# Kernel tuning notes

Measured on AMD Instinct MI355X. Metric: run time of the kernel, lower is better.

The kernel has to match this reference:

```python
import jax, jax.numpy as jnp
import numpy as np

N = 100000
E = 1600000
D = 128      # in_features
H = 128      # mlp hidden = out_features
O = 128      # out_features
BN_EPS = 1e-5

def _bn_train(x, gamma, beta):
    # BatchNorm1d in training mode: batch stats over node axis, biased variance
    mu = jnp.mean(x, axis=0)
    var = jnp.mean((x - mu) ** 2, axis=0)
    return (x - mu) * jax.lax.rsqrt(var + BN_EPS) * gamma + beta

def setup_inputs() -> dict:
    key = jax.random.key(0)
    ks = jax.random.split(key, 8)
    h = jax.random.normal(ks[0], (N, D), dtype=jnp.float32)
    edge_src = jax.random.randint(ks[1], (E,), 0, N, dtype=jnp.int32)
    edge_dst = jax.random.randint(ks[2], (E,), 0, N, dtype=jnp.int32)
    s1 = 1.0 / np.sqrt(D)
    s2 = 1.0 / np.sqrt(H)
    W1 = jax.random.uniform(ks[3], (D, H), jnp.float32, -s1, s1)
    b1 = jax.random.uniform(ks[4], (H,), jnp.float32, -s1, s1)
    W2 = jax.random.uniform(ks[5], (H, O), jnp.float32, -s2, s2)
    b2 = jax.random.uniform(ks[6], (O,), jnp.float32, -s2, s2)
    return {
        "h": h, "edge_src": edge_src, "edge_dst": edge_dst,
        "W1": W1, "b1": b1, "g1": jnp.ones((H,), jnp.float32), "be1": jnp.zeros((H,), jnp.float32),
        "W2": W2, "b2": b2, "g2": jnp.ones((O,), jnp.float32), "be2": jnp.zeros((O,), jnp.float32),
        "eps": jnp.zeros((), jnp.float32),
    }

def reference(h, edge_src, edge_dst, W1, b1, g1, be1, W2, b2, g2, be2, eps):
    # spmm(Adj, h) == scatter-add of gathered neighbor features
    msgs = h[edge_src]                                   # [E, D] irregular gather
    pooled = jax.ops.segment_sum(msgs, edge_dst, num_segments=N)  # [N, D]
    pooled = pooled + (1.0 + eps) * h                    # eps combine
    # MLP (2 layers): Linear -> BN -> ReLU -> Linear
    x = jax.nn.relu(_bn_train(pooled @ W1 + b1, g1, be1))
    x = x @ W2 + b2
    # final BN + ReLU
    return jax.nn.relu(_bn_train(x, g2, be2))
```

## Files before the change

kernel.cpp:

```cpp
#include <hip/hip_runtime.h>
#include <hip/hip_bf16.h>
#include <stdint.h>

#define BN_EPS 1e-5f

typedef __attribute__((ext_vector_type(8)))  short bf16x8;
typedef __attribute__((ext_vector_type(16))) float f32x16;

static __device__ __forceinline__ float bflo2f(uint32_t p){
  union { uint32_t u; float f; } c; c.u = p << 16; return c.f;
}
static __device__ __forceinline__ float bfhi2f(uint32_t p){
  union { uint32_t u; float f; } c; c.u = p & 0xffff0000u; return c.f;
}
static __device__ __forceinline__ uint16_t f2bf(float f){
  union { float f; uint32_t u; } c; c.f = f;
  uint32_t u = c.u;
  return (uint16_t)((u + 0x7fffu + ((u >> 16) & 1u)) >> 16);
}
static __device__ __forceinline__ uint32_t pack2(float a, float b){
  return (uint32_t)f2bf(a) | ((uint32_t)f2bf(b) << 16);
}

__global__ void k_prep(const float* __restrict__ h, uint16_t* __restrict__ hb, int hblocks,
                       const float* __restrict__ W1, const float* __restrict__ W2,
                       uint16_t* __restrict__ Wt1, uint16_t* __restrict__ Wt2){
  if ((int)blockIdx.x < hblocks){
    int i = (blockIdx.x * 256 + threadIdx.x) * 8;
    float4 a = *(const float4*)(h + i);
    float4 b = *(const float4*)(h + i + 4);
    uint4 o;
    o.x = pack2(a.x, a.y); o.y = pack2(a.z, a.w);
    o.z = pack2(b.x, b.y); o.w = pack2(b.z, b.w);
    *(uint4*)(hb + i) = o;
    return;
  }
  int gid = (blockIdx.x - hblocks) * 256 + threadIdx.x;
  if (gid >= 4096) return;
  const float* Wf = (gid < 2048) ? W1 : W2;
  uint16_t* Wt = (gid < 2048) ? Wt1 : Wt2;
  int cid = gid & 2047;
  int nrow = cid >> 4;
  int c    = cid & 15;
  int k0 = c * 8;
  float e[8];
  #pragma unroll
  for (int j = 0; j < 8; ++j) e[j] = Wf[(k0 + j) * 128 + nrow];
  uint4 o;
  o.x = pack2(e[0], e[1]); o.y = pack2(e[2], e[3]);
  o.z = pack2(e[4], e[5]); o.w = pack2(e[6], e[7]);
  int cs = c ^ (nrow & 15);
  *(uint4*)(Wt + nrow * 128 + cs * 8) = o;
}

__global__ void k_bhist(const int* __restrict__ dst, int* __restrict__ M, int E, int NB){
  __shared__ int cnt[512];
  int t = threadIdx.x;
  cnt[t] = 0; cnt[t + 256] = 0;
  __syncthreads();
  int base = blockIdx.x * 4096;
  #pragma unroll 4
  for (int j = t; j < 4096; j += 256){
    int i = base + j;
    if (i < E) atomicAdd(&cnt[dst[i] >> 8], 1);
  }
  __syncthreads();
  size_t row = (size_t)blockIdx.x * NB;
  if (t < NB) M[row + t] = cnt[t];
  int t2 = t + 256;
  if (t2 < NB) M[row + t2] = cnt[t2];
}

__global__ void k_colscan(int* __restrict__ M, int* __restrict__ btot, int EB, int NB){
  __shared__ int s[256];
  int b = blockIdx.x, t = threadIdx.x;
  int i0 = 2 * t, i1 = 2 * t + 1;
  int v0 = (i0 < EB) ? M[(size_t)i0 * NB + b] : 0;
  int v1 = (i1 < EB) ? M[(size_t)i1 * NB + b] : 0;
  s[t] = v0 + v1;
  __syncthreads();
  for (int off = 1; off < 256; off <<= 1){
    int v = (t >= off) ? s[t - off] : 0;
    __syncthreads();
    s[t] += v;
    __syncthreads();
  }
  int excl = s[t] - (v0 + v1);
  if (i0 < EB) M[(size_t)i0 * NB + b] = excl;
  if (i1 < EB) M[(size_t)i1 * NB + b] = excl + v0;
  if (t == 255) btot[b] = s[255];
}

__global__ void k_bscan(const int* __restrict__ btot, int* __restrict__ bbase,
                        int* __restrict__ row_off, int NB, int n, int E){
  __shared__ int s[256];
  int t = threadIdx.x;
  int i0 = 2 * t, i1 = 2 * t + 1;
  int v0 = (i0 < NB) ? btot[i0] : 0;
  int v1 = (i1 < NB) ? btot[i1] : 0;
  s[t] = v0 + v1;
  __syncthreads();
  for (int off = 1; off < 256; off <<= 1){
    int v = (t >= off) ? s[t - off] : 0;
    __syncthreads();
    s[t] += v;
    __syncthreads();
  }
  int excl = s[t] - (v0 + v1);
  if (i0 < NB) bbase[i0] = excl;
  if (i1 < NB) bbase[i1] = excl + v0;
  if (t == 0){ bbase[NB] = E; row_off[n] = E; }
}

__global__ void k_bin(const int* __restrict__ src, const int* __restrict__ dst,
                      const int* __restrict__ M, const int* __restrict__ bbase,
                      uint2* __restrict__ binned, int E, int NB){
  __shared__ int comb[512];
  __shared__ int cur[512];
  int t = threadIdx.x;
  size_t row = (size_t)blockIdx.x * NB;
  if (t < NB) comb[t] = bbase[t] + M[row + t];
  int t2 = t + 256;
  if (t2 < NB) comb[t2] = bbase[t2] + M[row + t2];
  cur[t] = 0; cur[t + 256] = 0;
  __syncthreads();
  int base = blockIdx.x * 4096;
  #pragma unroll 4
  for (int j = t; j < 4096; j += 256){
    int i = base + j;
    if (i < E){
      int d = dst[i];
      int b = d >> 8;
      int r = atomicAdd(&cur[b], 1);
      binned[comb[b] + r] = make_uint2((unsigned)src[i], (unsigned)d);
    }
  }
}

__global__ void k_csr(const uint2* __restrict__ binned, const int* __restrict__ bbase,
                      int* __restrict__ row_off, int* __restrict__ col_idx, int n){
  __shared__ int cnt[256];
  __shared__ int off[256];
  __shared__ int cur[256];
  int b = blockIdx.x, t = threadIdx.x;
  int e0 = bbase[b], e1 = bbase[b + 1];
  int nb0 = b << 8;
  cnt[t] = 0; cur[t] = 0;
  __syncthreads();
  int m = e1 - e0;
  for (int j = t; j < m; j += 256) atomicAdd(&cnt[binned[e0 + j].y & 255], 1);
  __syncthreads();
  int v = cnt[t];
  off[t] = v;
  __syncthreads();
  for (int o = 1; o < 256; o <<= 1){
    int u = (t >= o) ? off[t - o] : 0;
    __syncthreads();
    off[t] += u;
    __syncthreads();
  }
  int excl = off[t] - v;
  __syncthreads();
  off[t] = excl;
  if (nb0 + t < n) row_off[nb0 + t] = e0 + excl;
  __syncthreads();
  for (int j = t; j < m; j += 256){
    uint2 p = binned[e0 + j];
    int dl = p.y & 255;
    int r = atomicAdd(&cur[dl], 1);
    col_idx[e0 + off[dl] + r] = (int)p.x;
  }
}

__global__ void k_gather(const uint16_t* __restrict__ hb, const int* __restrict__ row_off,
                         const int* __restrict__ col_idx, const float* __restrict__ eps_p,
                         uint16_t* __restrict__ Xb, int n){
  int node = (blockIdx.x << 2) + (threadIdx.x >> 6);
  int lane = threadIdx.x & 63;
  if (node >= n) return;
  int g = lane >> 4;
  int c = lane & 15;
  const uint4* hp4 = (const uint4*)hb;
  int j = row_off[node], jend = row_off[node + 1];
  float a0=0.f,a1=0.f,a2=0.f,a3=0.f,a4=0.f,a5=0.f,a6=0.f,a7=0.f;
  for (; j + 8 <= jend; j += 8){
    int sA = col_idx[j + g];
    int sB = col_idx[j + 4 + g];
    uint4 vA = hp4[(size_t)sA * 16 + c];
    uint4 vB = hp4[(size_t)sB * 16 + c];
    a0 += bflo2f(vA.x) + bflo2f(vB.x);
    a1 += bfhi2f(vA.x) + bfhi2f(vB.x);
    a2 += bflo2f(vA.y) + bflo2f(vB.y);
    a3 += bfhi2f(vA.y) + bfhi2f(vB.y);
    a4 += bflo2f(vA.z) + bflo2f(vB.z);
    a5 += bfhi2f(vA.z) + bfhi2f(vB.z);
    a6 += bflo2f(vA.w) + bflo2f(vB.w);
    a7 += bfhi2f(vA.w) + bfhi2f(vB.w);
  }
  for (; j + 4 <= jend; j += 4){
    int s = col_idx[j + g];
    uint4 v = hp4[(size_t)s * 16 + c];
    a0 += bflo2f(v.x); a1 += bfhi2f(v.x);
    a2 += bflo2f(v.y); a3 += bfhi2f(v.y);
    a4 += bflo2f(v.z); a5 += bfhi2f(v.z);
    a6 += bflo2f(v.w); a7 += bfhi2f(v.w);
  }
  int rem = jend - j;
  if (rem > 0){
    int jj = j + (g < rem ? g : rem - 1);
    float w = (g < rem) ? 1.f : 0.f;
    int s = col_idx[jj];
    uint4 v = hp4[(size_t)s * 16 + c];
    a0 = fmaf(w, bflo2f(v.x), a0); a1 = fmaf(w, bfhi2f(v.x), a1);
    a2 = fmaf(w, bflo2f(v.y), a2); a3 = fmaf(w, bfhi2f(v.y), a3);
    a4 = fmaf(w, bflo2f(v.z), a4); a5 = fmaf(w, bfhi2f(v.z), a5);
    a6 = fmaf(w, bflo2f(v.w), a6); a7 = fmaf(w, bfhi2f(v.w), a7);
  }
  a0 += __shfl_xor(a0, 16); a1 += __shfl_xor(a1, 16);
  a2 += __shfl_xor(a2, 16); a3 += __shfl_xor(a3, 16);
  a4 += __shfl_xor(a4, 16); a5 += __shfl_xor(a5, 16);
  a6 += __shfl_xor(a6, 16); a7 += __shfl_xor(a7, 16);
  a0 += __shfl_xor(a0, 32); a1 += __shfl_xor(a1, 32);
  a2 += __shfl_xor(a2, 32); a3 += __shfl_xor(a3, 32);
  a4 += __shfl_xor(a4, 32); a5 += __shfl_xor(a5, 32);
  a6 += __shfl_xor(a6, 32); a7 += __shfl_xor(a7, 32);
  if (g == 0){
    float ce = 1.0f + eps_p[0];
    uint4 vh = hp4[(size_t)node * 16 + c];
    a0 = fmaf(ce, bflo2f(vh.x), a0); a1 = fmaf(ce, bfhi2f(vh.x), a1);
    a2 = fmaf(ce, bflo2f(vh.y), a2); a3 = fmaf(ce, bfhi2f(vh.y), a3);
    a4 = fmaf(ce, bflo2f(vh.z), a4); a5 = fmaf(ce, bfhi2f(vh.z), a5);
    a6 = fmaf(ce, bflo2f(vh.w), a6); a7 = fmaf(ce, bfhi2f(vh.w), a7);
    uint4 o;
    o.x = pack2(a0, a1); o.y = pack2(a2, a3);
    o.z = pack2(a4, a5); o.w = pack2(a6, a7);
    *((uint4*)Xb + (size_t)node * 16 + c) = o;
  }
}

template<bool BN_IN>
__global__ __launch_bounds__(256, 3) void k_mgemm(
    const uint16_t* __restrict__ Ag, const uint16_t* __restrict__ Wt,
    const float* __restrict__ bias_f, const float* __restrict__ ABin,
    uint16_t* __restrict__ Yout, float* __restrict__ osum, float* __restrict__ osq, int n){
  __shared__ __align__(16) uint16_t Al[64 * 128];
  __shared__ __align__(16) uint16_t Wl[128 * 128];
  __shared__ float csum[128], csq[128];
  int tid = threadIdx.x;
  int rbase = blockIdx.x * 64;

  {
    const uint4* g = (const uint4*)Wt;
    uint4* d = (uint4*)Wl;
    #pragma unroll
    for (int i = 0; i < 8; ++i) d[tid + 256 * i] = g[tid + 256 * i];
  }
  #pragma unroll
  for (int i = 0; i < 4; ++i){
    int f = tid + 256 * i;
    int m = f >> 4, c = f & 15;
    int gr = rbase + m;
    uint4 v = make_uint4(0, 0, 0, 0);
    if (gr < n){
      v = *(const uint4*)(Ag + (size_t)gr * 128 + c * 8);
      if (BN_IN){
        int k0 = c * 8;
        float4 ka0 = *(const float4*)(ABin + k0);
        float4 ka1 = *(const float4*)(ABin + k0 + 4);
        float4 kb0 = *(const float4*)(ABin + 128 + k0);
        float4 kb1 = *(const float4*)(ABin + 128 + k0 + 4);
        float e0 = fmaxf(fmaf(bflo2f(v.x), ka0.x, kb0.x), 0.f);
        float e1 = fmaxf(fmaf(bfhi2f(v.x), ka0.y, kb0.y), 0.f);
        float e2 = fmaxf(fmaf(bflo2f(v.y), ka0.z, kb0.z), 0.f);
        float e3 = fmaxf(fmaf(bfhi2f(v.y), ka0.w, kb0.w), 0.f);
        float e4 = fmaxf(fmaf(bflo2f(v.z), ka1.x, kb1.x), 0.f);
        float e5 = fmaxf(fmaf(bfhi2f(v.z), ka1.y, kb1.y), 0.f);
        float e6 = fmaxf(fmaf(bflo2f(v.w), ka1.z, kb1.z), 0.f);
        float e7 = fmaxf(fmaf(bfhi2f(v.w), ka1.w, kb1.w), 0.f);
        v.x = pack2(e0, e1); v.y = pack2(e2, e3);
        v.z = pack2(e4, e5); v.w = pack2(e6, e7);
      }
    }
    *(uint4*)((char*)Al + m * 256 + ((c ^ (m & 15)) * 16)) = v;
  }
  if (tid < 128){ csum[tid] = 0.f; csq[tid] = 0.f; }
  __syncthreads();

  int lane = tid & 63;
  int w    = tid >> 6;
  int hi   = lane >> 5;
  int key  = lane & 15;
  int m0   = (w & 1) * 32;
  int n0   = (w >> 1) * 64;
  int mrow = m0 + (lane & 31);
  int nrow0 = n0 + (lane & 31);
  int nrow1 = nrow0 + 32;

  f32x16 acc0, acc1;
  #pragma unroll
  for (int i = 0; i < 16; ++i){ acc0[i] = 0.f; acc1[i] = 0.f; }

  const char* Ab = (const char*)Al;
  const char* Wb = (const char*)Wl;
  #pragma unroll
  for (int kt = 0; kt < 8; ++kt){
    int cs = ((2 * kt + hi) ^ key) * 16;
    bf16x8 a  = *(const bf16x8*)(Ab + mrow  * 256 + cs);
    bf16x8 b0 = *(const bf16x8*)(Wb + nrow0 * 256 + cs);
    bf16x8 b1 = *(const bf16x8*)(Wb + nrow1 * 256 + cs);
    acc0 = __builtin_amdgcn_mfma_f32_32x32x16_bf16(a, b0, acc0, 0, 0, 0);
    acc1 = __builtin_amdgcn_mfma_f32_32x32x16_bf16(a, b1, acc1, 0, 0, 0);
  }
  __syncthreads();

  uint16_t* Yl = Wl;
  float bias0 = bias_f[nrow0];
  float bias1 = bias_f[nrow1];
  float ps0 = 0.f, pq0 = 0.f, ps1 = 0.f, pq1 = 0.f;
  #pragma unroll
  for (int r = 0; r < 16; ++r){
    int row = m0 + (r & 3) + 8 * (r >> 2) + 4 * hi;
    bool valid = (rbase + row) < n;
    float y0 = acc0[r] + bias0;
    float y1 = acc1[r] + bias1;
    if (valid){
      ps0 += y0; pq0 += y0 * y0;
      ps1 += y1; pq1 += y1 * y1;
    }
    Yl[row * 128 + nrow0] = f2bf(y0);
    Yl[row * 128 + nrow1] = f2bf(y1);
  }
  atomicAdd(&csum[nrow0], ps0); atomicAdd(&csq[nrow0], pq0);
  atomicAdd(&csum[nrow1], ps1); atomicAdd(&csq[nrow1], pq1);
  __syncthreads();

  #pragma unroll
  for (int i = 0; i < 4; ++i){
    int id = tid + 256 * i;
    int row = id >> 4, c = id & 15;
    int gr = rbase + row;
    if (gr < n)
      *((uint4*)Yout + (size_t)gr * 16 + c) = *((const uint4*)Yl + id);
  }
  if (tid < 128){
    atomicAdd(&osum[tid], csum[tid]);
    atomicAdd(&osq[tid], csq[tid]);
  }
}

__global__ void k_bncoef(const float* __restrict__ sum, const float* __restrict__ sq,
                         const float* __restrict__ g, const float* __restrict__ be,
                         float* __restrict__ AB, float invN){
  int c = threadIdx.x;
  if (c < 128){
    float mu = sum[c] * invN;
    float var = sq[c] * invN - mu * mu;
    float A = g[c] * rsqrtf(var + BN_EPS);
    float B = be[c] - mu * A;
    AB[c] = A;
    AB[128 + c] = B;
  }
}

__global__ void k_final(const uint16_t* __restrict__ Y2b, const float* __restrict__ AB,
                        float* __restrict__ out, int total){
  int i = (blockIdx.x * 256 + threadIdx.x) * 4;
  if (i >= total) return;
  uint2 v = *(const uint2*)(Y2b + i);
  int c = i & 127;
  float4 a = *(const float4*)(AB + c);
  float4 b = *(const float4*)(AB + 128 + c);
  float4 o;
  o.x = fmaxf(fmaf(bflo2f(v.x), a.x, b.x), 0.f);
  o.y = fmaxf(fmaf(bfhi2f(v.x), a.y, b.y), 0.f);
  o.z = fmaxf(fmaf(bflo2f(v.y), a.z, b.z), 0.f);
  o.w = fmaxf(fmaf(bfhi2f(v.y), a.w, b.w), 0.f);
  *(float4*)(out + i) = o;
}

extern "C" void kernel_launch(void* const* d_in, const int* in_sizes, int n_in,
                              void* d_out, int out_size, void* d_ws, size_t ws_size,
                              hipStream_t stream){
  const float* h    = (const float*)d_in[0];
  const int*   esrc = (const int*)d_in[1];
  const int*   edst = (const int*)d_in[2];
  const float* W1   = (const float*)d_in[3];
  const float* b1   = (const float*)d_in[4];
  const float* g1   = (const float*)d_in[5];
  const float* be1  = (const float*)d_in[6];
  const float* W2   = (const float*)d_in[7];
  const float* b2   = (const float*)d_in[8];
  const float* g2   = (const float*)d_in[9];
  const float* be2  = (const float*)d_in[10];
  const float* eps  = (const float*)d_in[11];
  int n = in_sizes[0] / 128;
  int E = in_sizes[1];
  (void)n_in; (void)out_size; (void)ws_size;

  int NB = (n + 255) >> 8;
  int EB = (E + 4095) >> 12;

  char* ws = (char*)d_ws;
  size_t off = 0;
  auto alloc = [&](size_t bytes) -> void* {
    void* p = ws + off;
    off += (bytes + 511) & ~(size_t)511;
    return p;
  };
  size_t feat_b = (size_t)n * 128 * 2;
  uint16_t* B1   = (uint16_t*)alloc(feat_b);
  uint16_t* B2   = (uint16_t*)alloc(feat_b);
  int*   row_off = (int*)alloc((size_t)(n + 1) * 4);
  int*   col_idx = (int*)alloc((size_t)E * 4);
  int*   M       = (int*)alloc((size_t)EB * NB * 4);
  int*   btot    = (int*)alloc((size_t)(NB + 1) * 4);
  int*   bbase   = (int*)alloc((size_t)(NB + 1) * 4);
  float* stats   = (float*)alloc(512 * 4);
  float* AB1     = (float*)alloc(256 * 4);
  float* AB2     = (float*)alloc(256 * 4);
  uint16_t* Wt1  = (uint16_t*)alloc(128 * 128 * 2);
  uint16_t* Wt2  = (uint16_t*)alloc(128 * 128 * 2);
  float* sum1 = stats;        float* sq1 = stats + 128;
  float* sum2 = stats + 256;  float* sq2 = stats + 384;
  uint16_t* hb  = B1;
  uint2*   binned = (uint2*)B2;
  uint16_t* Xb  = B2;
  uint16_t* Y1b = B1;
  uint16_t* Y2b = B2;

  hipMemsetAsync(stats, 0, 512 * 4, stream);

  int total = n * 128;
  int hblocks = total / 8 / 256;
  k_prep<<<hblocks + 16, 256, 0, stream>>>(h, hb, hblocks, W1, W2, Wt1, Wt2);

  k_bhist  <<<EB, 256, 0, stream>>>(edst, M, E, NB);
  k_colscan<<<NB, 256, 0, stream>>>(M, btot, EB, NB);
  k_bscan  <<<1, 256, 0, stream>>>(btot, bbase, row_off, NB, n, E);
  k_bin    <<<EB, 256, 0, stream>>>(esrc, edst, M, bbase, binned, E, NB);
  k_csr    <<<NB, 256, 0, stream>>>(binned, bbase, row_off, col_idx, n);

  k_gather<<<(n + 3) / 4, 256, 0, stream>>>(hb, row_off, col_idx, eps, Xb, n);

  int gblocks = (n + 63) / 64;
  k_mgemm<false><<<gblocks, 256, 0, stream>>>(Xb, Wt1, b1, nullptr, Y1b, sum1, sq1, n);
  k_bncoef<<<1, 128, 0, stream>>>(sum1, sq1, g1, be1, AB1, 1.0f / (float)n);
  k_mgemm<true> <<<gblocks, 256, 0, stream>>>(Y1b, Wt2, b2, AB1, Y2b, sum2, sq2, n);
  k_bncoef<<<1, 128, 0, stream>>>(sum2, sq2, g2, be2, AB2, 1.0f / (float)n);

  k_final<<<(total / 4 + 255) / 256, 256, 0, stream>>>(Y2b, AB2, (float*)d_out, total);
}
```

Measured before the change: 361.0 us.

## Fuse CSR build into one persistent kernel with grid barriers, fold BN coefficients

Merges the five CSR-construction kernels into one kernel that separates its phases with a global atomic grid barrier. The BN coefficient kernels are removed and each GEMM/final block recomputes the coefficients in shared memory. The stats memset moves into k_prep, and the gather loop is unrolled to 16 edges per iteration for more memory-level parallelism. The goal is to cut launch overhead and tiny serial kernels. The grid barrier assumes all NG (~391) blocks are co-resident, which risks deadlock if occupancy is insufficient.

```diff
diff --git a/kernel.cpp b/kernel.cpp
--- a/kernel.cpp
+++ b/kernel.cpp
@@ -24,7 +24,16 @@
 
 __global__ void k_prep(const float* __restrict__ h, uint16_t* __restrict__ hb, int hblocks,
                        const float* __restrict__ W1, const float* __restrict__ W2,
-                       uint16_t* __restrict__ Wt1, uint16_t* __restrict__ Wt2){
+                       uint16_t* __restrict__ Wt1, uint16_t* __restrict__ Wt2,
+                       float* __restrict__ stats, int* __restrict__ bar){
+  if (blockIdx.x == gridDim.x - 1){
+    if (threadIdx.x < 128){
+      float4 z = make_float4(0.f, 0.f, 0.f, 0.f);
+      *(float4*)(stats + threadIdx.x * 4) = z;
+    } else if (threadIdx.x == 128){
+      *bar = 0;
+    }
+  }
   if ((int)blockIdx.x < hblocks){
     int i = (blockIdx.x * 256 + threadIdx.x) * 8;
     float4 a = *(const float4*)(h + i);
@@ -53,122 +62,131 @@
   *(uint4*)(Wt + nrow * 128 + cs * 8) = o;
 }
 
-__global__ void k_bhist(const int* __restrict__ dst, int* __restrict__ M, int E, int NB){
-  __shared__ int cnt[512];
-  int t = threadIdx.x;
-  cnt[t] = 0; cnt[t + 256] = 0;
+static __device__ __forceinline__ void gridbar(int* bar, int nblocks, int phase){
   __syncthreads();
-  int base = blockIdx.x * 4096;
-  #pragma unroll 4
-  for (int j = t; j < 4096; j += 256){
-    int i = base + j;
-    if (i < E) atomicAdd(&cnt[dst[i] >> 8], 1);
+  if (threadIdx.x == 0){
+    __hip_atomic_fetch_add(bar, 1, __ATOMIC_RELEASE, __HIP_MEMORY_SCOPE_AGENT);
+    int target = nblocks * phase;
+    while (__hip_atomic_load(bar, __ATOMIC_ACQUIRE, __HIP_MEMORY_SCOPE_AGENT) < target){
+      __builtin_amdgcn_s_sleep(8);
+    }
   }
   __syncthreads();
-  size_t row = (size_t)blockIdx.x * NB;
-  if (t < NB) M[row + t] = cnt[t];
-  int t2 = t + 256;
-  if (t2 < NB) M[row + t2] = cnt[t2];
-}
-
-__global__ void k_colscan(int* __restrict__ M, int* __restrict__ btot, int EB, int NB){
-  __shared__ int s[256];
+}
+
+__global__ __launch_bounds__(256, 4) void k_csr_all(
+    const int* __restrict__ src, const int* __restrict__ dst,
+    int* __restrict__ M, int* __restrict__ btot, int* __restrict__ bbase,
+    int* __restrict__ row_off, int* __restrict__ col_idx, uint2* __restrict__ binned,
+    int* __restrict__ bar, int E, int n, int NB, int EB, int NG){
+  __shared__ int sm[1024];
   int b = blockIdx.x, t = threadIdx.x;
-  int i0 = 2 * t, i1 = 2 * t + 1;
-  int v0 = (i0 < EB) ? M[(size_t)i0 * NB + b] : 0;
-  int v1 = (i1 < EB) ? M[(size_t)i1 * NB + b] : 0;
-  s[t] = v0 + v1;
-  __syncthreads();
-  for (int off = 1; off < 256; off <<= 1){
-    int v = (t >= off) ? s[t - off] : 0;
-    __syncthreads();
-    s[t] += v;
-    __syncthreads();
-  }
-  int excl = s[t] - (v0 + v1);
-  if (i0 < EB) M[(size_t)i0 * NB + b] = excl;
-  if (i1 < EB) M[(size_t)i1 * NB + b] = excl + v0;
-  if (t == 255) btot[b] = s[255];
-}
-
-__global__ void k_bscan(const int* __restrict__ btot, int* __restrict__ bbase,
-                        int* __restrict__ row_off, int NB, int n, int E){
-  __shared__ int s[256];
-  int t = threadIdx.x;
-  int i0 = 2 * t, i1 = 2 * t + 1;
-  int v0 = (i0 < NB) ? btot[i0] : 0;
-  int v1 = (i1 < NB) ? btot[i1] : 0;
-  s[t] = v0 + v1;
-  __syncthreads();
-  for (int off = 1; off < 256; off <<= 1){
-    int v = (t >= off) ? s[t - off] : 0;
-    __syncthreads();
-    s[t] += v;
-    __syncthreads();
-  }
-  int excl = s[t] - (v0 + v1);
-  if (i0 < NB) bbase[i0] = excl;
-  if (i1 < NB) bbase[i1] = excl + v0;
-  if (t == 0){ bbase[NB] = E; row_off[n] = E; }
-}
-
-__global__ void k_bin(const int* __restrict__ src, const int* __restrict__ dst,
-                      const int* __restrict__ M, const int* __restrict__ bbase,
-                      uint2* __restrict__ binned, int E, int NB){
-  __shared__ int comb[512];
-  __shared__ int cur[512];
-  int t = threadIdx.x;
-  size_t row = (size_t)blockIdx.x * NB;
-  if (t < NB) comb[t] = bbase[t] + M[row + t];
-  int t2 = t + 256;
-  if (t2 < NB) comb[t2] = bbase[t2] + M[row + t2];
-  cur[t] = 0; cur[t + 256] = 0;
-  __syncthreads();
-  int base = blockIdx.x * 4096;
-  #pragma unroll 4
-  for (int j = t; j < 4096; j += 256){
-    int i = base + j;
-    if (i < E){
-      int d = dst[i];
-      int b = d >> 8;
-      int r = atomicAdd(&cur[b], 1);
-      binned[comb[b] + r] = make_uint2((unsigned)src[i], (unsigned)d);
-    }
-  }
-}
-
-__global__ void k_csr(const uint2* __restrict__ binned, const int* __restrict__ bbase,
-                      int* __restrict__ row_off, int* __restrict__ col_idx, int n){
-  __shared__ int cnt[256];
-  __shared__ int off[256];
-  __shared__ int cur[256];
-  int b = blockIdx.x, t = threadIdx.x;
-  int e0 = bbase[b], e1 = bbase[b + 1];
-  int nb0 = b << 8;
-  cnt[t] = 0; cur[t] = 0;
-  __syncthreads();
-  int m = e1 - e0;
-  for (int j = t; j < m; j += 256) atomicAdd(&cnt[binned[e0 + j].y & 255], 1);
-  __syncthreads();
-  int v = cnt[t];
-  off[t] = v;
-  __syncthreads();
-  for (int o = 1; o < 256; o <<= 1){
-    int u = (t >= o) ? off[t - o] : 0;
-    __syncthreads();
-    off[t] += u;
-    __syncthreads();
-  }
-  int excl = off[t] - v;
-  __syncthreads();
-  off[t] = excl;
-  if (nb0 + t < n) row_off[nb0 + t] = e0 + excl;
-  __syncthreads();
-  for (int j = t; j < m; j += 256){
-    uint2 p = binned[e0 + j];
-    int dl = p.y & 255;
-    int r = atomicAdd(&cur[dl], 1);
-    col_idx[e0 + off[dl] + r] = (int)p.x;
+
+  if (b < EB){
+    sm[t] = 0; sm[t + 256] = 0;
+    __syncthreads();
+    int base = b * 4096;
+    #pragma unroll 4
+    for (int j = t; j < 4096; j += 256){
+      int i = base + j;
+      if (i < E) atomicAdd(&sm[dst[i] >> 8], 1);
+    }
+    __syncthreads();
+    size_t row = (size_t)b * NB;
+    if (t < NB) M[row + t] = sm[t];
+    int t2 = t + 256;
+    if (t2 < NB) M[row + t2] = sm[t2];
+  }
+  gridbar(bar, NG, 1);
+
+  if (b < NB){
+    int i0 = 2 * t, i1 = 2 * t + 1;
+    int v0 = (i0 < EB) ? M[(size_t)i0 * NB + b] : 0;
+    int v1 = (i1 < EB) ? M[(size_t)i1 * NB + b] : 0;
+    sm[t] = v0 + v1;
+    __syncthreads();
+    for (int off = 1; off < 256; off <<= 1){
+      int v = (t >= off) ? sm[t - off] : 0;
+      __syncthreads();
+      sm[t] += v;
+      __syncthreads();
+    }
+    int excl = sm[t] - (v0 + v1);
+    if (i0 < EB) M[(size_t)i0 * NB + b] = excl;
+    if (i1 < EB) M[(size_t)i1 * NB + b] = excl + v0;
+    if (t == 255) btot[b] = sm[255];
+  }
+  gridbar(bar, NG, 2);
+
+  if (b == 0){
+    int i0 = 2 * t, i1 = 2 * t + 1;
+    int v0 = (i0 < NB) ? btot[i0] : 0;
+    int v1 = (i1 < NB) ? btot[i1] : 0;
+    sm[t] = v0 + v1;
+    __syncthreads();
+    for (int off = 1; off < 256; off <<= 1){
+      int v = (t >= off) ? sm[t - off] : 0;
+      __syncthreads();
+      sm[t] += v;
+      __syncthreads();
+    }
+    int excl = sm[t] - (v0 + v1);
+    if (i0 < NB) bbase[i0] = excl;
+    if (i1 < NB) bbase[i1] = excl + v0;
+    if (t == 0){ bbase[NB] = E; row_off[n] = E; }
+  }
+  gridbar(bar, NG, 3);
+
+  if (b < EB){
+    size_t row = (size_t)b * NB;
+    if (t < NB) sm[t] = bbase[t] + M[row + t];
+    int t2 = t + 256;
+    if (t2 < NB) sm[t2] = bbase[t2] + M[row + t2];
+    sm[512 + t] = 0; sm[768 + t] = 0;
+    __syncthreads();
+    int base = b * 4096;
+    #pragma unroll 4
+    for (int j = t; j < 4096; j += 256){
+      int i = base + j;
+      if (i < E){
+        int d = dst[i];
+        int bk = d >> 8;
+        int r = atomicAdd(&sm[512 + bk], 1);
+        binned[sm[bk] + r] = make_uint2((unsigned)src[i], (unsigned)d);
+      }
+    }
+  }
+  gridbar(bar, NG, 4);
+
+  if (b < NB){
+    int e0 = bbase[b], e1 = bbase[b + 1];
+    int nb0 = b << 8;
+    sm[t] = 0;
+    sm[512 + t] = 0;
+    __syncthreads();
+    int m = e1 - e0;
+    for (int j = t; j < m; j += 256) atomicAdd(&sm[binned[e0 + j].y & 255], 1);
+    __syncthreads();
+    int v = sm[t];
+    sm[256 + t] = v;
+    __syncthreads();
+    for (int o = 1; o < 256; o <<= 1){
+      int u = (t >= o) ? sm[256 + t - o] : 0;
+      __syncthreads();
+      sm[256 + t] += u;
+      __syncthreads();
+    }
+    int excl = sm[256 + t] - v;
+    __syncthreads();
+    sm[256 + t] = excl;
+    if (nb0 + t < n) row_off[nb0 + t] = e0 + excl;
+    __syncthreads();
+    for (int j = t; j < m; j += 256){
+      uint2 p = binned[e0 + j];
+      int dl = p.y & 255;
+      int r = atomicAdd(&sm[512 + dl], 1);
+      col_idx[e0 + sm[256 + dl] + r] = (int)p.x;
+    }
   }
 }
 
@@ -183,6 +201,24 @@
   const uint4* hp4 = (const uint4*)hb;
   int j = row_off[node], jend = row_off[node + 1];
   float a0=0.f,a1=0.f,a2=0.f,a3=0.f,a4=0.f,a5=0.f,a6=0.f,a7=0.f;
+  for (; j + 16 <= jend; j += 16){
+    int sA = col_idx[j + g];
+    int sB = col_idx[j + 4 + g];
+    int sC = col_idx[j + 8 + g];
+    int sD = col_idx[j + 12 + g];
+    uint4 vA = hp4[(size_t)sA * 16 + c];
+    uint4 vB = hp4[(size_t)sB * 16 + c];
+    uint4 vC = hp4[(size_t)sC * 16 + c];
+    uint4 vD = hp4[(size_t)sD * 16 + c];
+    a0 += (bflo2f(vA.x) + bflo2f(vB.x)) + (bflo2f(vC.x) + bflo2f(vD.x));
+    a1 += (bfhi2f(vA.x) + bfhi2f(vB.x)) + (bfhi2f(vC.x) + bfhi2f(vD.x));
+    a2 += (bflo2f(vA.y) + bflo2f(vB.y)) + (bflo2f(vC.y) + bflo2f(vD.y));
+    a3 += (bfhi2f(vA.y) + bfhi2f(vB.y)) + (bfhi2f(vC.y) + bfhi2f(vD.y));
+    a4 += (bflo2f(vA.z) + bflo2f(vB.z)) + (bflo2f(vC.z) + bflo2f(vD.z));
+    a5 += (bfhi2f(vA.z) + bfhi2f(vB.z)) + (bfhi2f(vC.z) + bfhi2f(vD.z));
+    a6 += (bflo2f(vA.w) + bflo2f(vB.w)) + (bflo2f(vC.w) + bflo2f(vD.w));
+    a7 += (bfhi2f(vA.w) + bfhi2f(vB.w)) + (bfhi2f(vC.w) + bfhi2f(vD.w));
+  }
   for (; j + 8 <= jend; j += 8){
     int sA = col_idx[j + g];
     int sB = col_idx[j + 4 + g];
@@ -241,13 +277,27 @@
 template<bool BN_IN>
 __global__ __launch_bounds__(256, 3) void k_mgemm(
     const uint16_t* __restrict__ Ag, const uint16_t* __restrict__ Wt,
-    const float* __restrict__ bias_f, const float* __restrict__ ABin,
+    const float* __restrict__ bias_f,
+    const float* __restrict__ sin, const float* __restrict__ sqin,
+    const float* __restrict__ gin, const float* __restrict__ bein, float invN,
     uint16_t* __restrict__ Yout, float* __restrict__ osum, float* __restrict__ osq, int n){
   __shared__ __align__(16) uint16_t Al[64 * 128];
   __shared__ __align__(16) uint16_t Wl[128 * 128];
   __shared__ float csum[128], csq[128];
+  __shared__ __align__(16) float ABl[256];
   int tid = threadIdx.x;
   int rbase = blockIdx.x * 64;
+
+  if (BN_IN){
+    if (tid < 128){
+      float mu = sin[tid] * invN;
+      float var = sqin[tid] * invN - mu * mu;
+      float A = gin[tid] * rsqrtf(var + BN_EPS);
+      ABl[tid] = A;
+      ABl[128 + tid] = bein[tid] - mu * A;
+    }
+    __syncthreads();
+  }
 
   {
     const uint4* g = (const uint4*)Wt;
@@ -265,10 +315,10 @@
       v = *(const uint4*)(Ag + (size_t)gr * 128 + c * 8);
       if (BN_IN){
         int k0 = c * 8;
-        float4 ka0 = *(const float4*)(ABin + k0);
-        float4 ka1 = *(const float4*)(ABin + k0 + 4);
-        float4 kb0 = *(const float4*)(ABin + 128 + k0);
-        float4 kb1 = *(const float4*)(ABin + 128 + k0 + 4);
+        float4 ka0 = *(const float4*)(ABl + k0);
+        float4 ka1 = *(const float4*)(ABl + k0 + 4);
+        float4 kb0 = *(const float4*)(ABl + 128 + k0);
+        float4 kb1 = *(const float4*)(ABl + 128 + k0 + 4);
         float e0 = fmaxf(fmaf(bflo2f(v.x), ka0.x, kb0.x), 0.f);
         float e1 = fmaxf(fmaf(bfhi2f(v.x), ka0.y, kb0.y), 0.f);
         float e2 = fmaxf(fmaf(bflo2f(v.y), ka0.z, kb0.z), 0.f);
@@ -348,23 +398,21 @@
   }
 }
 
-__global__ void k_bncoef(const float* __restrict__ sum, const float* __restrict__ sq,
-                         const float* __restrict__ g, const float* __restrict__ be,
-                         float* __restrict__ AB, float invN){
-  int c = threadIdx.x;
-  if (c < 128){
-    float mu = sum[c] * invN;
-    float var = sq[c] * invN - mu * mu;
-    float A = g[c] * rsqrtf(var + BN_EPS);
-    float B = be[c] - mu * A;
-    AB[c] = A;
-    AB[128 + c] = B;
-  }
-}
-
-__global__ void k_final(const uint16_t* __restrict__ Y2b, const float* __restrict__ AB,
+__global__ void k_final(const uint16_t* __restrict__ Y2b,
+                        const float* __restrict__ sum2, const float* __restrict__ sq2,
+                        const float* __restrict__ g2, const float* __restrict__ be2, float invN,
                         float* __restrict__ out, int total){
-  int i = (blockIdx.x * 256 + threadIdx.x) * 4;
+  __shared__ __align__(16) float AB[256];
+  int tid = threadIdx.x;
+  if (tid < 128){
+    float mu = sum2[tid] * invN;
+    float var = sq2[tid] * invN - mu * mu;
+    float A = g2[tid] * rsqrtf(var + BN_EPS);
+    AB[tid] = A;
+    AB[128 + tid] = be2[tid] - mu * A;
+  }
+  __syncthreads();
+  int i = (blockIdx.x * 256 + tid) * 4;
   if (i >= total) return;
   uint2 v = *(const uint2*)(Y2b + i);
   int c = i & 127;
@@ -399,6 +447,7 @@
 
   int NB = (n + 255) >> 8;
   int EB = (E + 4095) >> 12;
+  int NG = (EB > NB) ? EB : NB;
 
   char* ws = (char*)d_ws;
   size_t off = 0;
@@ -416,10 +465,11 @@
   int*   btot    = (int*)alloc((size_t)(NB + 1) * 4);
   int*   bbase   = (int*)alloc((size_t)(NB + 1) * 4);
   float* stats   = (float*)alloc(512 * 4);
+  int*   bar     = (int*)alloc(64 * 4);
   float* AB1     = (float*)alloc(256 * 4);
-  float* AB2     = (float*)alloc(256 * 4);
   uint16_t* Wt1  = (uint16_t*)alloc(128 * 128 * 2);
   uint16_t* Wt2  = (uint16_t*)alloc(128 * 128 * 2);
+  (void)AB1;
   float* sum1 = stats;        float* sq1 = stats + 128;
   float* sum2 = stats + 256;  float* sq2 = stats + 384;
   uint16_t* hb  = B1;
@@ -428,25 +478,23 @@
   uint16_t* Y1b = B1;
   uint16_t* Y2b = B2;
 
-  hipMemsetAsync(stats, 0, 512 * 4, stream);
-
   int total = n * 128;
   int hblocks = total / 8 / 256;
-  k_prep<<<hblocks + 16, 256, 0, stream>>>(h, hb, hblocks, W1, W2, Wt1, Wt2);
-
-  k_bhist  <<<EB, 256, 0, stream>>>(edst, M, E, NB);
-  k_colscan<<<NB, 256, 0, stream>>>(M, btot, EB, NB);
-  k_bscan  <<<1, 256, 0, stream>>>(btot, bbase, row_off, NB, n, E);
-  k_bin    <<<EB, 256, 0, stream>>>(esrc, edst, M, bbase, binned, E, NB);
-  k_csr    <<<NB, 256, 0, stream>>>(binned, bbase, row_off, col_idx, n);
+  float invN = 1.0f / (float)n;
+
+  k_prep<<<hblocks + 16, 256, 0, stream>>>(h, hb, hblocks, W1, W2, Wt1, Wt2, stats, bar);
+
+  k_csr_all<<<NG, 256, 0, stream>>>(esrc, edst, M, btot, bbase, row_off, col_idx,
+                                    binned, bar, E, n, NB, EB, NG);
 
   k_gather<<<(n + 3) / 4, 256, 0, stream>>>(hb, row_off, col_idx, eps, Xb, n);
 
   int gblocks = (n + 63) / 64;
-  k_mgemm<false><<<gblocks, 256, 0, stream>>>(Xb, Wt1, b1, nullptr, Y1b, sum1, sq1, n);
-  k_bncoef<<<1, 128, 0, stream>>>(sum1, sq1, g1, be1, AB1, 1.0f / (float)n);
-  k_mgemm<true> <<<gblocks, 256, 0, stream>>>(Y1b, Wt2, b2, AB1, Y2b, sum2, sq2, n);
-  k_bncoef<<<1, 128, 0, stream>>>(sum2, sq2, g2, be2, AB2, 1.0f / (float)n);
-
-  k_final<<<(total / 4 + 255) / 256, 256, 0, stream>>>(Y2b, AB2, (float*)d_out, total);
-}
+  k_mgemm<false><<<gblocks, 256, 0, stream>>>(Xb, Wt1, b1,
+      nullptr, nullptr, nullptr, nullptr, 0.f, Y1b, sum1, sq1, n);
+  k_mgemm<true> <<<gblocks, 256, 0, stream>>>(Y1b, Wt2, b2,
+      sum1, sq1, g1, be1, invN, Y2b, sum2, sq2, n);
+
+  k_final<<<(total / 4 + 255) / 256, 256, 0, stream>>>(Y2b, sum2, sq2, g2, be2, invN,
+                                                       (float*)d_out, total);
+}
```

Result: slower. 527.1 us (+46.0%).

## Merge small launches: fold histogram and memset into prep, BN coefs into consumers

Applied to the files above, without the earlier changes.

Merges the edge-histogram kernel and the stats memset into the prep kernel, and computes the BatchNorm coefficients inside the second GEMM and the final kernel instead of in separate single-block launches. It also adds a 16-edge unrolled path to the gather loop for more memory-level parallelism. The aim is to cut launch count and serialization gaps between tiny kernels. In exchange, every block now recomputes the coefficients redundantly, and the prep kernel mixes heterogeneous block types.

```diff
diff --git a/kernel.cpp b/kernel.cpp
--- a/kernel.cpp
+++ b/kernel.cpp
@@ -24,48 +24,55 @@
 
 __global__ void k_prep(const float* __restrict__ h, uint16_t* __restrict__ hb, int hblocks,
                        const float* __restrict__ W1, const float* __restrict__ W2,
-                       uint16_t* __restrict__ Wt1, uint16_t* __restrict__ Wt2){
-  if ((int)blockIdx.x < hblocks){
-    int i = (blockIdx.x * 256 + threadIdx.x) * 8;
+                       uint16_t* __restrict__ Wt1, uint16_t* __restrict__ Wt2,
+                       float* __restrict__ stats,
+                       const int* __restrict__ dst, int* __restrict__ M, int E, int NB){
+  int b = blockIdx.x, t = threadIdx.x;
+  if (b < hblocks){
+    int i = (b * 256 + t) * 8;
     float4 a = *(const float4*)(h + i);
-    float4 b = *(const float4*)(h + i + 4);
+    float4 bb = *(const float4*)(h + i + 4);
     uint4 o;
     o.x = pack2(a.x, a.y); o.y = pack2(a.z, a.w);
-    o.z = pack2(b.x, b.y); o.w = pack2(b.z, b.w);
+    o.z = pack2(bb.x, bb.y); o.w = pack2(bb.z, bb.w);
     *(uint4*)(hb + i) = o;
     return;
   }
-  int gid = (blockIdx.x - hblocks) * 256 + threadIdx.x;
-  if (gid >= 4096) return;
-  const float* Wf = (gid < 2048) ? W1 : W2;
-  uint16_t* Wt = (gid < 2048) ? Wt1 : Wt2;
-  int cid = gid & 2047;
-  int nrow = cid >> 4;
-  int c    = cid & 15;
-  int k0 = c * 8;
-  float e[8];
-  #pragma unroll
-  for (int j = 0; j < 8; ++j) e[j] = Wf[(k0 + j) * 128 + nrow];
-  uint4 o;
-  o.x = pack2(e[0], e[1]); o.y = pack2(e[2], e[3]);
-  o.z = pack2(e[4], e[5]); o.w = pack2(e[6], e[7]);
-  int cs = c ^ (nrow & 15);
-  *(uint4*)(Wt + nrow * 128 + cs * 8) = o;
-}
-
-__global__ void k_bhist(const int* __restrict__ dst, int* __restrict__ M, int E, int NB){
+  if (b < hblocks + 16){
+    if (b == hblocks && t < 128){
+      float4 z = make_float4(0.f, 0.f, 0.f, 0.f);
+      *(float4*)(stats + t * 4) = z;
+    }
+    int gid = (b - hblocks) * 256 + t;
+    if (gid >= 4096) return;
+    const float* Wf = (gid < 2048) ? W1 : W2;
+    uint16_t* Wt = (gid < 2048) ? Wt1 : Wt2;
+    int cid = gid & 2047;
+    int nrow = cid >> 4;
+    int c    = cid & 15;
+    int k0 = c * 8;
+    float e[8];
+    #pragma unroll
+    for (int j = 0; j < 8; ++j) e[j] = Wf[(k0 + j) * 128 + nrow];
+    uint4 o;
+    o.x = pack2(e[0], e[1]); o.y = pack2(e[2], e[3]);
+    o.z = pack2(e[4], e[5]); o.w = pack2(e[6], e[7]);
+    int cs = c ^ (nrow & 15);
+    *(uint4*)(Wt + nrow * 128 + cs * 8) = o;
+    return;
+  }
+  int eb = b - hblocks - 16;
   __shared__ int cnt[512];
-  int t = threadIdx.x;
   cnt[t] = 0; cnt[t + 256] = 0;
   __syncthreads();
-  int base = blockIdx.x * 4096;
+  int base = eb * 4096;
   #pragma unroll 4
   for (int j = t; j < 4096; j += 256){
     int i = base + j;
     if (i < E) atomicAdd(&cnt[dst[i] >> 8], 1);
   }
   __syncthreads();
-  size_t row = (size_t)blockIdx.x * NB;
+  size_t row = (size_t)eb * NB;
   if (t < NB) M[row + t] = cnt[t];
   int t2 = t + 256;
   if (t2 < NB) M[row + t2] = cnt[t2];
@@ -183,6 +190,24 @@
   const uint4* hp4 = (const uint4*)hb;
   int j = row_off[node], jend = row_off[node + 1];
   float a0=0.f,a1=0.f,a2=0.f,a3=0.f,a4=0.f,a5=0.f,a6=0.f,a7=0.f;
+  for (; j + 16 <= jend; j += 16){
+    int sA = col_idx[j + g];
+    int sB = col_idx[j + 4 + g];
+    int sC = col_idx[j + 8 + g];
+    int sD = col_idx[j + 12 + g];
+    uint4 vA = hp4[(size_t)sA * 16 + c];
+    uint4 vB = hp4[(size_t)sB * 16 + c];
+    uint4 vC = hp4[(size_t)sC * 16 + c];
+    uint4 vD = hp4[(size_t)sD * 16 + c];
+    a0 += (bflo2f(vA.x) + bflo2f(vB.x)) + (bflo2f(vC.x) + bflo2f(vD.x));
+    a1 += (bfhi2f(vA.x) + bfhi2f(vB.x)) + (bfhi2f(vC.x) + bfhi2f(vD.x));
+    a2 += (bflo2f(vA.y) + bflo2f(vB.y)) + (bflo2f(vC.y) + bflo2f(vD.y));
+    a3 += (bfhi2f(vA.y) + bfhi2f(vB.y)) + (bfhi2f(vC.y) + bfhi2f(vD.y));
+    a4 += (bflo2f(vA.z) + bflo2f(vB.z)) + (bflo2f(vC.z) + bflo2f(vD.z));
+    a5 += (bfhi2f(vA.z) + bfhi2f(vB.z)) + (bfhi2f(vC.z) + bfhi2f(vD.z));
+    a6 += (bflo2f(vA.w) + bflo2f(vB.w)) + (bflo2f(vC.w) + bflo2f(vD.w));
+    a7 += (bfhi2f(vA.w) + bfhi2f(vB.w)) + (bfhi2f(vC.w) + bfhi2f(vD.w));
+  }
   for (; j + 8 <= jend; j += 8){
     int sA = col_idx[j + g];
     int sB = col_idx[j + 4 + g];
@@ -241,13 +266,27 @@
 template<bool BN_IN>
 __global__ __launch_bounds__(256, 3) void k_mgemm(
     const uint16_t* __restrict__ Ag, const uint16_t* __restrict__ Wt,
-    const float* __restrict__ bias_f, const float* __restrict__ ABin,
+    const float* __restrict__ bias_f,
+    const float* __restrict__ sin, const float* __restrict__ sqin,
+    const float* __restrict__ gin, const float* __restrict__ bein, float invN,
     uint16_t* __restrict__ Yout, float* __restrict__ osum, float* __restrict__ osq, int n){
   __shared__ __align__(16) uint16_t Al[64 * 128];
   __shared__ __align__(16) uint16_t Wl[128 * 128];
   __shared__ float csum[128], csq[128];
+  __shared__ __align__(16) float ABl[256];
   int tid = threadIdx.x;
   int rbase = blockIdx.x * 64;
+
+  if (BN_IN){
+    if (tid < 128){
+      float mu = sin[tid] * invN;
+      float var = sqin[tid] * invN - mu * mu;
+      float A = gin[tid] * rsqrtf(var + BN_EPS);
+      ABl[tid] = A;
+      ABl[128 + tid] = bein[tid] - mu * A;
+    }
+    __syncthreads();
+  }
 
   {
     const uint4* g = (const uint4*)Wt;
@@ -265,10 +304,10 @@
       v = *(const uint4*)(Ag + (size_t)gr * 128 + c * 8);
       if (BN_IN){
         int k0 = c * 8;
-        float4 ka0 = *(const float4*)(ABin + k0);
-        float4 ka1 = *(const float4*)(ABin + k0 + 4);
-        float4 kb0 = *(const float4*)(ABin + 128 + k0);
-        float4 kb1 = *(const float4*)(ABin + 128 + k0 + 4);
+        float4 ka0 = *(const float4*)(ABl + k0);
+        float4 ka1 = *(const float4*)(ABl + k0 + 4);
+        float4 kb0 = *(const float4*)(ABl + 128 + k0);
+        float4 kb1 = *(const float4*)(ABl + 128 + k0 + 4);
         float e0 = fmaxf(fmaf(bflo2f(v.x), ka0.x, kb0.x), 0.f);
         float e1 = fmaxf(fmaf(bfhi2f(v.x), ka0.y, kb0.y), 0.f);
         float e2 = fmaxf(fmaf(bflo2f(v.y), ka0.z, kb0.z), 0.f);
@@ -348,23 +387,21 @@
   }
 }
 
-__global__ void k_bncoef(const float* __restrict__ sum, const float* __restrict__ sq,
-                         const float* __restrict__ g, const float* __restrict__ be,
-                         float* __restrict__ AB, float invN){
-  int c = threadIdx.x;
-  if (c < 128){
-    float mu = sum[c] * invN;
-    float var = sq[c] * invN - mu * mu;
-    float A = g[c] * rsqrtf(var + BN_EPS);
-    float B = be[c] - mu * A;
-    AB[c] = A;
-    AB[128 + c] = B;
-  }
-}
-
-__global__ void k_final(const uint16_t* __restrict__ Y2b, const float* __restrict__ AB,
+__global__ void k_final(const uint16_t* __restrict__ Y2b,
+                        const float* __restrict__ sum2, const float* __restrict__ sq2,
+                        const float* __restrict__ g2, const float* __restrict__ be2, float invN,
                         float* __restrict__ out, int total){
-  int i = (blockIdx.x * 256 + threadIdx.x) * 4;
+  __shared__ __align__(16) float AB[256];
+  int tid = threadIdx.x;
+  if (tid < 128){
+    float mu = sum2[tid] * invN;
+    float var = sq2[tid] * invN - mu * mu;
+    float A = g2[tid] * rsqrtf(var + BN_EPS);
+    AB[tid] = A;
+    AB[128 + tid] = be2[tid] - mu * A;
+  }
+  __syncthreads();
+  int i = (blockIdx.x * 256 + tid) * 4;
   if (i >= total) return;
   uint2 v = *(const uint2*)(Y2b + i);
   int c = i & 127;
@@ -416,8 +453,6 @@
   int*   btot    = (int*)alloc((size_t)(NB + 1) * 4);
   int*   bbase   = (int*)alloc((size_t)(NB + 1) * 4);
   float* stats   = (float*)alloc(512 * 4);
-  float* AB1     = (float*)alloc(256 * 4);
-  float* AB2     = (float*)alloc(256 * 4);
   uint16_t* Wt1  = (uint16_t*)alloc(128 * 128 * 2);
   uint16_t* Wt2  = (uint16_t*)alloc(128 * 128 * 2);
   float* sum1 = stats;        float* sq1 = stats + 128;
@@ -428,13 +463,12 @@
   uint16_t* Y1b = B1;
   uint16_t* Y2b = B2;
 
-  hipMemsetAsync(stats, 0, 512 * 4, stream);
-
   int total = n * 128;
   int hblocks = total / 8 / 256;
-  k_prep<<<hblocks + 16, 256, 0, stream>>>(h, hb, hblocks, W1, W2, Wt1, Wt2);
-
-  k_bhist  <<<EB, 256, 0, stream>>>(edst, M, E, NB);
+  float invN = 1.0f / (float)n;
+
+  k_prep<<<hblocks + 16 + EB, 256, 0, stream>>>(h, hb, hblocks, W1, W2, Wt1, Wt2,
+                                                stats, edst, M, E, NB);
   k_colscan<<<NB, 256, 0, stream>>>(M, btot, EB, NB);
   k_bscan  <<<1, 256, 0, stream>>>(btot, bbase, row_off, NB, n, E);
   k_bin    <<<EB, 256, 0, stream>>>(esrc, edst, M, bbase, binned, E, NB);
@@ -443,10 +477,11 @@
   k_gather<<<(n + 3) / 4, 256, 0, stream>>>(hb, row_off, col_idx, eps, Xb, n);
 
   int gblocks = (n + 63) / 64;
-  k_mgemm<false><<<gblocks, 256, 0, stream>>>(Xb, Wt1, b1, nullptr, Y1b, sum1, sq1, n);
-  k_bncoef<<<1, 128, 0, stream>>>(sum1, sq1, g1, be1, AB1, 1.0f / (float)n);
-  k_mgemm<true> <<<gblocks, 256, 0, stream>>>(Y1b, Wt2, b2, AB1, Y2b, sum2, sq2, n);
-  k_bncoef<<<1, 128, 0, stream>>>(sum2, sq2, g2, be2, AB2, 1.0f / (float)n);
-
-  k_final<<<(total / 4 + 255) / 256, 256, 0, stream>>>(Y2b, AB2, (float*)d_out, total);
-}
+  k_mgemm<false><<<gblocks, 256, 0, stream>>>(Xb, Wt1, b1,
+      nullptr, nullptr, nullptr, nullptr, 0.f, Y1b, sum1, sq1, n);
+  k_mgemm<true> <<<gblocks, 256, 0, stream>>>(Y1b, Wt2, b2,
+      sum1, sq1, g1, be1, invN, Y2b, sum2, sq2, n);
+
+  k_final<<<(total / 4 + 255) / 256, 256, 0, stream>>>(Y2b, sum2, sq2, g2, be2, invN,
+                                                       (float*)d_out, total);
+}
```

New measurement: 354.4 us. No clear change (-1.8%).
